# Performance work log

Hardware: AMD Instinct MI355X
Metric: run time of the kernel (lower is better)

The kernel has to match this reference:

```python
import jax, jax.numpy as jnp
import numpy as np

N = 50000
E = 1600000
NUM_GRAPHS = 64
NEG_SLOPE = 0.2


def _glorot(key, shape):
    fan_in, fan_out = shape[0], shape[-1]
    lim = jnp.sqrt(6.0 / (fan_in + fan_out))
    return jax.random.uniform(key, shape, jnp.float32, -lim, lim)


def setup_inputs() -> dict:
    key = jax.random.key(0)
    ks = jax.random.split(key, 16)
    x = jax.random.normal(ks[0], (N, 128), jnp.float32)
    edge_index = jax.random.randint(ks[1], (2, E), 0, N, jnp.int64)
    batch = jnp.sort(jax.random.randint(ks[2], (N,), 0, NUM_GRAPHS, jnp.int64))
    dims = [(128, 32), (32, 64), (64, 128)]
    params = {}
    for i, (fi, fo) in enumerate(dims, start=1):
        params[f'W{i}'] = _glorot(ks[3 * i], (fi, fo))
        params[f'a_src{i}'] = _glorot(ks[3 * i + 1], (1, fo))[0]
        params[f'a_dst{i}'] = _glorot(ks[3 * i + 2], (1, fo))[0]
        params[f'b{i}'] = jnp.zeros((fo,), jnp.float32)
    params['lin1_W'] = _glorot(ks[12], (128, 32))
    params['lin1_b'] = jnp.zeros((32,), jnp.float32)
    params['lin2_W'] = _glorot(ks[13], (32, 10))
    params['lin2_b'] = jnp.zeros((10,), jnp.float32)
    return dict(x=x, edge_index=edge_index, batch=batch, **params)


def gat_conv(x, src, dst, W, a_src, a_dst, b):
    # h: [N, F_out]
    h = x @ W
    # per-node attention logits, gathered per edge
    as_n = h @ a_src  # [N]
    ad_n = h @ a_dst  # [N]
    e = jax.nn.leaky_relu(as_n[src] + ad_n[dst], NEG_SLOPE)  # [E']
    # segment softmax over incoming edges of each destination node
    m = jax.ops.segment_max(e, dst, num_segments=N)
    ee = jnp.exp(e - m[dst])
    s = jax.ops.segment_sum(ee, dst, num_segments=N)
    alpha = ee / (s[dst] + 1e-16)
    # weighted scatter-add of source messages
    out = jax.ops.segment_sum(h[src] * alpha[:, None], dst, num_segments=N)
    return out + b


def reference(x, edge_index, batch, W1, a_src1, a_dst1, b1, W2, a_src2, a_dst2, b2,
              W3, a_src3, a_dst3, b3, lin1_W, lin1_b, lin2_W, lin2_b):
    # add self loops (PyG GATConv default)
    loops = jnp.arange(N, dtype=edge_index.dtype)
    src = jnp.concatenate([edge_index[0], loops])
    dst = jnp.concatenate([edge_index[1], loops])
    h = jax.nn.relu(gat_conv(x, src, dst, W1, a_src1, a_dst1, b1))
    h = jax.nn.relu(gat_conv(h, src, dst, W2, a_src2, a_dst2, b2))
    h = gat_conv(h, src, dst, W3, a_src3, a_dst3, b3)
    # global_add_pool over graphs
    g = jax.ops.segment_sum(h, batch, num_segments=NUM_GRAPHS)  # [G, 128]
    g = jax.nn.relu(g @ lin1_W + lin1_b)
    g = g @ lin2_W + lin2_b
    # faithful to original: log_softmax over dim=0 (batch axis)
    return jax.nn.log_softmax(g, axis=0)
```

## Files before the change

### kernel.cpp

```cpp
#include <hip/hip_runtime.h>
#include <cstdint>
#include <cstddef>

#define NN 50000
#define NE 1600000
#define NG 64
#define NCB 391
#define HB 98
#define EPB_A 8192
#define CAP_B 8192

__device__ __forceinline__ float bflo(unsigned u) { return __uint_as_float(u << 16); }
__device__ __forceinline__ float bfhi(unsigned u) { return __uint_as_float(u & 0xffff0000u); }
__device__ __forceinline__ unsigned f2bf(float f) {
    unsigned u = __float_as_uint(f);
    return (u + 0x7fffu + ((u >> 16) & 1u)) >> 16;
}
__device__ __forceinline__ float rdlane_f(float v, int l) {
    return __uint_as_float((unsigned)__builtin_amdgcn_readlane((int)__float_as_uint(v), l));
}

template <int FIN, int FOUT, bool HIST, bool ABF16>
__global__ void gemm_att_k(const void* __restrict__ Ain, const float* __restrict__ W,
                           const float* __restrict__ a_src, const float* __restrict__ a_dst,
                           unsigned* __restrict__ Hb, float* __restrict__ as_,
                           float* __restrict__ ad_, int gemmBlocks,
                           const int* __restrict__ edst, int* __restrict__ gcount) {
    __shared__ float Wl[FIN * FOUT];
    __shared__ float Al[32 * FIN];
    __shared__ int hh[NCB];
    int tid = threadIdx.x;
    if (HIST && blockIdx.x >= gemmBlocks) {
        int bid = blockIdx.x - gemmBlocks;
        for (int i = tid; i < NCB; i += 256) hh[i] = 0;
        __syncthreads();
        const int total4 = NE / 4;
        for (int i = bid * 256 + tid; i < total4; i += HB * 256) {
            int4 d = ((const int4*)edst)[i];
            atomicAdd(&hh[d.x >> 7], 1);
            atomicAdd(&hh[d.y >> 7], 1);
            atomicAdd(&hh[d.z >> 7], 1);
            atomicAdd(&hh[d.w >> 7], 1);
        }
        __syncthreads();
        for (int i = tid; i < NCB; i += 256)
            if (hh[i]) atomicAdd(&gcount[i], hh[i]);
        return;
    }
    const int RPB = 32;
    const int CP = FOUT / 2;
    const int CLANES = 256 / CP;
    const int RL = RPB / CLANES;
    for (int i = tid; i < (FIN * FOUT) / 4; i += 256)
        ((float4*)Wl)[i] = ((const float4*)W)[i];
    int rowbase = blockIdx.x * RPB;
    int nrows = min(RPB, NN - rowbase);
    int nel4 = (nrows * FIN) / 4;
    if (ABF16) {
        const ushort4* As = (const ushort4*)Ain + (size_t)rowbase * (FIN / 4);
        for (int i = tid; i < nel4; i += 256) {
            ushort4 u = As[i];
            ((float4*)Al)[i] = make_float4(bflo((unsigned)u.x), bflo((unsigned)u.y),
                                           bflo((unsigned)u.z), bflo((unsigned)u.w));
        }
    } else {
        const float4* As = (const float4*)Ain + (size_t)rowbase * (FIN / 4);
        for (int i = tid; i < nel4; i += 256) ((float4*)Al)[i] = As[i];
    }
    __syncthreads();
    int c2 = tid % CP;
    int rb = tid / CP;
    float acc0[RL], acc1[RL];
#pragma unroll
    for (int r = 0; r < RL; ++r) { acc0[r] = 0.f; acc1[r] = 0.f; }
#pragma unroll 4
    for (int k = 0; k < FIN; ++k) {
        float w0 = Wl[k * FOUT + 2 * c2];
        float w1 = Wl[k * FOUT + 2 * c2 + 1];
#pragma unroll
        for (int r = 0; r < RL; ++r) {
            float a = Al[(rb + r * CLANES) * FIN + k];
            acc0[r] += a * w0;
            acc1[r] += a * w1;
        }
    }
    float2 asrc2 = ((const float2*)a_src)[c2];
    float2 adst2 = ((const float2*)a_dst)[c2];
#pragma unroll
    for (int r = 0; r < RL; ++r) {
        int row = rowbase + rb + r * CLANES;
        float p1 = acc0[r] * asrc2.x + acc1[r] * asrc2.y;
        float p2 = acc0[r] * adst2.x + acc1[r] * adst2.y;
#pragma unroll
        for (int o = CP >> 1; o; o >>= 1) {
            p1 += __shfl_xor(p1, o, CP);
            p2 += __shfl_xor(p2, o, CP);
        }
        if (row < NN) {
            Hb[(size_t)row * CP + c2] = f2bf(acc0[r]) | (f2bf(acc1[r]) << 16);
            if (c2 == 0) { as_[row] = p1; ad_[row] = p2; }
        }
    }
}

__global__ void cscan_k(const int* __restrict__ gcount, int* __restrict__ cbase,
                        int* __restrict__ gcur) {
    __shared__ int part[256];
    int tid = threadIdx.x;
    int i0 = 2 * tid, i1 = 2 * tid + 1;
    int v0 = (i0 < NCB) ? gcount[i0] : 0;
    int v1 = (i1 < NCB) ? gcount[i1] : 0;
    part[tid] = v0 + v1;
    __syncthreads();
    for (int off = 1; off < 256; off <<= 1) {
        int v = (tid >= off) ? part[tid - off] : 0;
        __syncthreads();
        part[tid] += v;
        __syncthreads();
    }
    int run = tid ? part[tid - 1] : 0;
    if (i0 < NCB) { cbase[i0] = run; gcur[i0] = run; run += v0; }
    if (i1 < NCB) { cbase[i1] = run; gcur[i1] = run; run += v1; }
    if (tid == 255) cbase[NCB] = part[255];
}

__global__ void parta_k(const int* __restrict__ esrc, const int* __restrict__ edst,
                        int* __restrict__ gcur, int* __restrict__ pk_g) {
    __shared__ int cnt[NCB];
    __shared__ int base[NCB];
    __shared__ int cur[NCB];
    __shared__ int gposs[NCB];
    __shared__ int sc[256];
    __shared__ int lpk[EPB_A];
    int tid = threadIdx.x;
    int e0 = blockIdx.x * EPB_A;
    int e1 = min(e0 + EPB_A, NE);
    for (int i = tid; i < NCB; i += 256) cnt[i] = 0;
    __syncthreads();
    for (int i = e0 / 4 + tid; i < e1 / 4; i += 256) {
        int4 d = ((const int4*)edst)[i];
        atomicAdd(&cnt[d.x >> 7], 1);
        atomicAdd(&cnt[d.y >> 7], 1);
        atomicAdd(&cnt[d.z >> 7], 1);
        atomicAdd(&cnt[d.w >> 7], 1);
    }
    __syncthreads();
    int i0 = 2 * tid, i1 = 2 * tid + 1;
    int c0 = (i0 < NCB) ? cnt[i0] : 0;
    int c1 = (i1 < NCB) ? cnt[i1] : 0;
    sc[tid] = c0 + c1;
    __syncthreads();
    for (int off = 1; off < 256; off <<= 1) {
        int v = (tid >= off) ? sc[tid - off] : 0;
        __syncthreads();
        sc[tid] += v;
        __syncthreads();
    }
    int run = tid ? sc[tid - 1] : 0;
    if (i0 < NCB) {
        base[i0] = run; cur[i0] = run;
        gposs[i0] = atomicAdd(&gcur[i0], c0);
        run += c0;
    }
    if (i1 < NCB) {
        base[i1] = run; cur[i1] = run;
        gposs[i1] = atomicAdd(&gcur[i1], c1);
        run += c1;
    }
    __syncthreads();
    for (int i = e0 / 4 + tid; i < e1 / 4; i += 256) {
        int4 d = ((const int4*)edst)[i];
        int4 s = ((const int4*)esrc)[i];
        lpk[atomicAdd(&cur[d.x >> 7], 1)] = s.x | ((d.x & 127) << 17);
        lpk[atomicAdd(&cur[d.y >> 7], 1)] = s.y | ((d.y & 127) << 17);
        lpk[atomicAdd(&cur[d.z >> 7], 1)] = s.z | ((d.z & 127) << 17);
        lpk[atomicAdd(&cur[d.w >> 7], 1)] = s.w | ((d.w & 127) << 17);
    }
    __syncthreads();
    int wid = tid >> 6, lane = tid & 63;
    for (int c = wid; c < NCB; c += 4) {
        int n = cnt[c], gb = gposs[c], lb = base[c];
        for (int i = lane; i < n; i += 64) pk_g[gb + i] = lpk[lb + i];
    }
}

__global__ void partb_k(const int* __restrict__ pk_g, const int* __restrict__ cbase,
                        int* __restrict__ offsets, int* __restrict__ csr) {
    __shared__ int cnt[128];
    __shared__ int sc[256];
    __shared__ int lpk[CAP_B];
    int b = blockIdx.x, tid = threadIdx.x;
    int ebeg = cbase[b], eend = cbase[b + 1], n = eend - ebeg;
    int nbeg = b * 128;
    int ncnt = min(128, NN - nbeg);
    if (tid < 128) cnt[tid] = 0;
    __syncthreads();
    bool fits = (n <= CAP_B);
    if (fits) {
        for (int i = tid; i < n; i += 256) {
            int p = pk_g[ebeg + i];
            lpk[i] = p;
            atomicAdd(&cnt[p >> 17], 1);
        }
    } else {
        for (int i = tid; i < n; i += 256) atomicAdd(&cnt[pk_g[ebeg + i] >> 17], 1);
    }
    __syncthreads();
    int c0 = (tid < 128) ? cnt[tid] : 0;
    sc[tid] = c0;
    __syncthreads();
    for (int off = 1; off < 128; off <<= 1) {
        int v = (tid >= off && tid < 128) ? sc[tid - off] : 0;
        __syncthreads();
        if (tid < 128) sc[tid] += v;
        __syncthreads();
    }
    int excl = (tid < 128) ? sc[tid] - c0 : 0;
    if (tid < ncnt) offsets[nbeg + tid] = ebeg + excl;
    if (b == NCB - 1 && tid == 0) offsets[NN] = eend;
    __syncthreads();
    if (tid < 128) cnt[tid] = ebeg + excl;
    __syncthreads();
    if (fits) {
        for (int i = tid; i < n; i += 256) {
            int p = lpk[i];
            csr[atomicAdd(&cnt[p >> 17], 1)] = p & 0x1FFFF;
        }
    } else {
        for (int i = tid; i < n; i += 256) {
            int p = pk_g[ebeg + i];
            csr[atomicAdd(&cnt[p >> 17], 1)] = p & 0x1FFFF;
        }
    }
}

template <int F, bool RELU>
__global__ void node_agg_k(const int* __restrict__ off, const int* __restrict__ csr,
                           const float* __restrict__ as_, const float* __restrict__ ad_,
                           const unsigned* __restrict__ Hb2,
                           const float* __restrict__ b, unsigned* __restrict__ Ob) {
    int lane = threadIdx.x;
    int node = blockIdx.x;
    int beg = off[node], end = off[node + 1];
    float adn = ad_[node];
    float vself = as_[node] + adn;
    vself = vself > 0.f ? vself : 0.2f * vself;
    float eself = __expf(vself);
    float lsum = 0.f;

    if constexpr (F == 128) {
        unsigned hbs = Hb2[(size_t)node * 64 + lane];
        float accx = eself * bflo(hbs);
        float accy = eself * bfhi(hbs);
        for (int i0 = beg; i0 < end; i0 += 64) {
            int idx = i0 + lane;
            bool ok = idx < end;
            int s = ok ? csr[idx] : 0;
            float v = as_[s] + adn;
            v = v > 0.f ? v : 0.2f * v;
            float ee = ok ? __expf(v) : 0.f;
            lsum += ee;
            int rem = min(end - i0, 64);
            int j = 0;
            for (; j + 16 <= rem; j += 16) {
#pragma unroll
                for (int k = 0; k < 16; ++k) {
                    int s2 = __builtin_amdgcn_readlane(s, j + k);
                    float ee2 = rdlane_f(ee, j + k);
                    unsigned hb = (Hb2 + (size_t)s2 * 64)[lane];
                    accx += ee2 * bflo(hb);
                    accy += ee2 * bfhi(hb);
                }
            }
            for (; j + 4 <= rem; j += 4) {
#pragma unroll
                for (int k = 0; k < 4; ++k) {
                    int s2 = __builtin_amdgcn_readlane(s, j + k);
                    float ee2 = rdlane_f(ee, j + k);
                    unsigned hb = (Hb2 + (size_t)s2 * 64)[lane];
                    accx += ee2 * bflo(hb);
                    accy += ee2 * bfhi(hb);
                }
            }
            for (; j < rem; ++j) {
                int s2 = __builtin_amdgcn_readlane(s, j);
                float ee2 = rdlane_f(ee, j);
                unsigned hb = (Hb2 + (size_t)s2 * 64)[lane];
                accx += ee2 * bflo(hb);
                accy += ee2 * bfhi(hb);
            }
        }
#pragma unroll
        for (int o = 32; o; o >>= 1) lsum += __shfl_xor(lsum, o);
        float inv = 1.f / (lsum + eself + 1e-16f);
        float2 bb = ((const float2*)b)[lane];
        float ox = accx * inv + bb.x;
        float oy = accy * inv + bb.y;
        if (RELU) { ox = fmaxf(ox, 0.f); oy = fmaxf(oy, 0.f); }
        Ob[(size_t)node * 64 + lane] = f2bf(ox) | (f2bf(oy) << 16);
    } else if constexpr (F == 64) {
        int sg = lane >> 5;
        int cl = lane & 31;
        unsigned hbs = Hb2[(size_t)node * 32 + cl];
        float accx = (sg == 0) ? eself * bflo(hbs) : 0.f;
        float accy = (sg == 0) ? eself * bfhi(hbs) : 0.f;
        for (int i0 = beg; i0 < end; i0 += 64) {
            int idx = i0 + lane;
            bool ok = idx < end;
            int s = ok ? csr[idx] : 0;
            float v = as_[s] + adn;
            v = v > 0.f ? v : 0.2f * v;
            float ee = ok ? __expf(v) : 0.f;
            lsum += ee;
            int rem = min(end - i0, 64);
            int nj = (rem + 1) >> 1;
            nj = (nj + 3) & ~3;
            for (int j = 0; j < nj; j += 4) {
#pragma unroll
                for (int k = 0; k < 4; ++k) {
                    int pos = (j + k) * 2 + sg;
                    int s2 = __shfl(s, pos);
                    float ee2 = __shfl(ee, pos);
                    unsigned hb = Hb2[(size_t)s2 * 32 + cl];
                    accx += ee2 * bflo(hb);
                    accy += ee2 * bfhi(hb);
                }
            }
        }
#pragma unroll
        for (int o = 32; o; o >>= 1) lsum += __shfl_xor(lsum, o);
        float sum = lsum + eself;
        accx += __shfl_xor(accx, 32);
        accy += __shfl_xor(accy, 32);
        if (sg == 0) {
            float inv = 1.f / (sum + 1e-16f);
            float2 bb = ((const float2*)b)[cl];
            float ox = accx * inv + bb.x;
            float oy = accy * inv + bb.y;
            if (RELU) { ox = fmaxf(ox, 0.f); oy = fmaxf(oy, 0.f); }
            Ob[(size_t)node * 32 + cl] = f2bf(ox) | (f2bf(oy) << 16);
        }
    } else {
        const int GRP = 16, EPG = 4, U = 4;
        int sg = lane / GRP;
        int cl = lane % GRP;
        unsigned hbs = Hb2[(size_t)node * GRP + cl];
        float accx = (sg == 0) ? eself * bflo(hbs) : 0.f;
        float accy = (sg == 0) ? eself * bfhi(hbs) : 0.f;
        for (int i0 = beg; i0 < end; i0 += 64) {
            int idx = i0 + lane;
            bool ok = idx < end;
            int s = ok ? csr[idx] : 0;
            float v = as_[s] + adn;
            v = v > 0.f ? v : 0.2f * v;
            float ee = ok ? __expf(v) : 0.f;
            lsum += ee;
            int rem = min(end - i0, 64);
            int nj = (rem + EPG - 1) / EPG;
            nj = (nj + U - 1) & ~(U - 1);
            for (int j = 0; j < nj; j += U) {
#pragma unroll
                for (int k = 0; k < U; ++k) {
                    int pos = (j + k) * EPG + sg;
                    int s2 = __shfl(s, pos);
                    float ee2 = __shfl(ee, pos);
                    unsigned hb = Hb2[(size_t)s2 * GRP + cl];
                    accx += ee2 * bflo(hb);
                    accy += ee2 * bfhi(hb);
                }
            }
        }
#pragma unroll
        for (int o = 32; o; o >>= 1) lsum += __shfl_xor(lsum, o);
        float sum = lsum + eself;
#pragma unroll
        for (int o = 32; o >= GRP; o >>= 1) {
            accx += __shfl_xor(accx, o);
            accy += __shfl_xor(accy, o);
        }
        if (sg == 0) {
            float inv = 1.f / (sum + 1e-16f);
            float2 bb = ((const float2*)b)[cl];
            float ox = accx * inv + bb.x;
            float oy = accy * inv + bb.y;
            if (RELU) { ox = fmaxf(ox, 0.f); oy = fmaxf(oy, 0.f); }
            Ob[(size_t)node * GRP + cl] = f2bf(ox) | (f2bf(oy) << 16);
        }
    }
}

__global__ void pool_k(const unsigned* __restrict__ Ob, const int* __restrict__ batch,
                       float* __restrict__ g, int nodes_per_block) {
    __shared__ float acc[NG * 128];
    int c2 = threadIdx.x;
    for (int i = 0; i < NG; ++i) {
        acc[i * 128 + 2 * c2] = 0.f;
        acc[i * 128 + 2 * c2 + 1] = 0.f;
    }
    int start = blockIdx.x * nodes_per_block;
    int end = min(start + nodes_per_block, NN);
    int gmin = NG - 1, gmax = 0;
    for (int nd = start; nd < end; ++nd) {
        int gg = batch[nd];
        gmin = min(gmin, gg);
        gmax = max(gmax, gg);
        unsigned hb = Ob[(size_t)nd * 64 + c2];
        acc[gg * 128 + 2 * c2] += bflo(hb);
        acc[gg * 128 + 2 * c2 + 1] += bfhi(hb);
    }
    for (int i = gmin; i <= gmax; ++i) {
        atomicAdd(g + i * 128 + 2 * c2, acc[i * 128 + 2 * c2]);
        atomicAdd(g + i * 128 + 2 * c2 + 1, acc[i * 128 + 2 * c2 + 1]);
    }
}

__global__ void head_k(const float* __restrict__ g, const float* __restrict__ l1W,
                       const float* __restrict__ l1b, const float* __restrict__ l2W,
                       const float* __restrict__ l2b, float* __restrict__ out) {
    __shared__ float h1[NG * 32];
    __shared__ float o[NG * 10];
    int tid = threadIdx.x;
    for (int idx = tid; idx < NG * 32; idx += 256) {
        int r = idx / 32, c = idx % 32;
        float acc = l1b[c];
        for (int k = 0; k < 128; ++k) acc += g[r * 128 + k] * l1W[k * 32 + c];
        h1[idx] = fmaxf(acc, 0.f);
    }
    __syncthreads();
    for (int idx = tid; idx < NG * 10; idx += 256) {
        int r = idx / 10, c = idx % 10;
        float acc = l2b[c];
        for (int k = 0; k < 32; ++k) acc += h1[r * 32 + k] * l2W[k * 10 + c];
        o[idx] = acc;
    }
    __syncthreads();
    if (tid < 10) {
        float mx = -1e30f;
        for (int r = 0; r < NG; ++r) mx = fmaxf(mx, o[r * 10 + tid]);
        float sum = 0.f;
        for (int r = 0; r < NG; ++r) sum += __expf(o[r * 10 + tid] - mx);
        float lse = mx + logf(sum);
        for (int r = 0; r < NG; ++r) out[r * 10 + tid] = o[r * 10 + tid] - lse;
    }
}

extern "C" void kernel_launch(void* const* d_in, const int* in_sizes, int n_in,
                              void* d_out, int out_size, void* d_ws, size_t ws_size,
                              hipStream_t stream) {
    const float* x   = (const float*)d_in[0];
    const int* ei    = (const int*)d_in[1];
    const int* batch = (const int*)d_in[2];
    const float* W1 = (const float*)d_in[3];
    const float* as1 = (const float*)d_in[4];
    const float* ad1 = (const float*)d_in[5];
    const float* b1 = (const float*)d_in[6];
    const float* W2 = (const float*)d_in[7];
    const float* as2 = (const float*)d_in[8];
    const float* ad2 = (const float*)d_in[9];
    const float* b2 = (const float*)d_in[10];
    const float* W3 = (const float*)d_in[11];
    const float* as3 = (const float*)d_in[12];
    const float* ad3 = (const float*)d_in[13];
    const float* b3 = (const float*)d_in[14];
    const float* l1W = (const float*)d_in[15];
    const float* l1b = (const float*)d_in[16];
    const float* l2W = (const float*)d_in[17];
    const float* l2b = (const float*)d_in[18];
    float* out = (float*)d_out;

    const int* esrc = ei;
    const int* edst = ei + NE;

    char* ws = (char*)d_ws;
    unsigned* Hb  = (unsigned*)ws;
    unsigned* B0b = Hb + (size_t)NN * 64;
    unsigned* B1b = B0b + (size_t)NN * 16;
    unsigned* B2b = B1b + (size_t)NN * 32;
    float* as_ = (float*)(B2b + (size_t)NN * 64);
    float* ad_ = as_ + NN;
    int* gcount = (int*)(ad_ + NN);
    float* g    = (float*)(gcount + NCB);
    int* cbase  = (int*)(g + NG * 128);
    int* gcur   = cbase + NCB + 1;
    int* offsets = gcur + NCB + 2;
    int* csr    = offsets + NN + 1;
    int* pk     = csr + NE;
    const int GEMM_BLOCKS = (NN + 31) / 32;

    hipMemsetAsync(gcount, 0, (NCB + NG * 128) * 4, stream);

    gemm_att_k<128, 32, true, false><<<GEMM_BLOCKS + HB, 256, 0, stream>>>(
        x, W1, as1, ad1, Hb, as_, ad_, GEMM_BLOCKS, edst, gcount);
    cscan_k<<<1, 256, 0, stream>>>(gcount, cbase, gcur);
    parta_k<<<(NE + EPB_A - 1) / EPB_A, 256, 0, stream>>>(esrc, edst, gcur, pk);
    partb_k<<<NCB, 256, 0, stream>>>(pk, cbase, offsets, csr);
    node_agg_k<32, true><<<NN, 64, 0, stream>>>(offsets, csr, as_, ad_, Hb, b1, B0b);

    gemm_att_k<32, 64, false, true><<<GEMM_BLOCKS, 256, 0, stream>>>(
        B0b, W2, as2, ad2, Hb, as_, ad_, GEMM_BLOCKS, nullptr, nullptr);
    node_agg_k<64, true><<<NN, 64, 0, stream>>>(offsets, csr, as_, ad_, Hb, b2, B1b);

    gemm_att_k<64, 128, false, true><<<GEMM_BLOCKS, 256, 0, stream>>>(
        B1b, W3, as3, ad3, Hb, as_, ad_, GEMM_BLOCKS, nullptr, nullptr);
    node_agg_k<128, false><<<NN, 64, 0, stream>>>(offsets, csr, as_, ad_, Hb, b3, B2b);

    pool_k<<<(NN + 127) / 128, 64, 0, stream>>>(B2b, batch, g, 128);
    head_k<<<1, 256, 0, stream>>>(g, l1W, l1b, l2W, l2b, out);
}
```

Before: 291.3 us.

## Fuse next-layer GEMM and attention projections into node aggregation epilogue

The layer-2 and layer-3 dense transforms and their attention logits are now computed in the epilogue of the previous layer's per-node aggregation kernel. Each wavefront multiplies its aggregated row by the next weight matrix and writes the bf16 features plus the src/dst logits directly. This drops two GEMM launches and the round trip of the intermediate activations through global memory. In exchange, every node block reads the full weight matrix from global or cache instead of shared memory, and the per-node epilogue becomes heavier, with double-buffered logit arrays to avoid read/write hazards.

```diff
diff --git a/kernel.cpp b/kernel.cpp
--- a/kernel.cpp
+++ b/kernel.cpp
@@ -20,8 +20,8 @@
     return __uint_as_float((unsigned)__builtin_amdgcn_readlane((int)__float_as_uint(v), l));
 }
 
-template <int FIN, int FOUT, bool HIST, bool ABF16>
-__global__ void gemm_att_k(const void* __restrict__ Ain, const float* __restrict__ W,
+template <int FIN, int FOUT, bool HIST>
+__global__ void gemm_att_k(const float* __restrict__ Ain, const float* __restrict__ W,
                            const float* __restrict__ a_src, const float* __restrict__ a_dst,
                            unsigned* __restrict__ Hb, float* __restrict__ as_,
                            float* __restrict__ ad_, int gemmBlocks,
@@ -56,17 +56,8 @@
     int rowbase = blockIdx.x * RPB;
     int nrows = min(RPB, NN - rowbase);
     int nel4 = (nrows * FIN) / 4;
-    if (ABF16) {
-        const ushort4* As = (const ushort4*)Ain + (size_t)rowbase * (FIN / 4);
-        for (int i = tid; i < nel4; i += 256) {
-            ushort4 u = As[i];
-            ((float4*)Al)[i] = make_float4(bflo((unsigned)u.x), bflo((unsigned)u.y),
-                                           bflo((unsigned)u.z), bflo((unsigned)u.w));
-        }
-    } else {
-        const float4* As = (const float4*)Ain + (size_t)rowbase * (FIN / 4);
-        for (int i = tid; i < nel4; i += 256) ((float4*)Al)[i] = As[i];
-    }
+    const float4* As = (const float4*)Ain + (size_t)rowbase * (FIN / 4);
+    for (int i = tid; i < nel4; i += 256) ((float4*)Al)[i] = As[i];
     __syncthreads();
     int c2 = tid % CP;
     int rb = tid / CP;
@@ -234,29 +225,32 @@
     }
 }
 
-template <int F, bool RELU>
+template <int F, bool FUSE>
 __global__ void node_agg_k(const int* __restrict__ off, const int* __restrict__ csr,
-                           const float* __restrict__ as_, const float* __restrict__ ad_,
-                           const unsigned* __restrict__ Hb2,
-                           const float* __restrict__ b, unsigned* __restrict__ Ob) {
+                           const float* __restrict__ as_in, const float* __restrict__ ad_in,
+                           const unsigned* __restrict__ Hb_in, const float* __restrict__ b,
+                           unsigned* __restrict__ Ob,
+                           const float* __restrict__ Wn, const float* __restrict__ an_src,
+                           const float* __restrict__ an_dst, unsigned* __restrict__ Hb_out,
+                           float* __restrict__ as_out, float* __restrict__ ad_out) {
     int lane = threadIdx.x;
     int node = blockIdx.x;
     int beg = off[node], end = off[node + 1];
-    float adn = ad_[node];
-    float vself = as_[node] + adn;
+    float adn = ad_in[node];
+    float vself = as_in[node] + adn;
     vself = vself > 0.f ? vself : 0.2f * vself;
     float eself = __expf(vself);
     float lsum = 0.f;
 
     if constexpr (F == 128) {
-        unsigned hbs = Hb2[(size_t)node * 64 + lane];
+        unsigned hbs = Hb_in[(size_t)node * 64 + lane];
         float accx = eself * bflo(hbs);
         float accy = eself * bfhi(hbs);
         for (int i0 = beg; i0 < end; i0 += 64) {
             int idx = i0 + lane;
             bool ok = idx < end;
             int s = ok ? csr[idx] : 0;
-            float v = as_[s] + adn;
+            float v = as_in[s] + adn;
             v = v > 0.f ? v : 0.2f * v;
             float ee = ok ? __expf(v) : 0.f;
             lsum += ee;
@@ -267,7 +261,7 @@
                 for (int k = 0; k < 16; ++k) {
                     int s2 = __builtin_amdgcn_readlane(s, j + k);
                     float ee2 = rdlane_f(ee, j + k);
-                    unsigned hb = (Hb2 + (size_t)s2 * 64)[lane];
+                    unsigned hb = (Hb_in + (size_t)s2 * 64)[lane];
                     accx += ee2 * bflo(hb);
                     accy += ee2 * bfhi(hb);
                 }
@@ -277,7 +271,7 @@
                 for (int k = 0; k < 4; ++k) {
                     int s2 = __builtin_amdgcn_readlane(s, j + k);
                     float ee2 = rdlane_f(ee, j + k);
-                    unsigned hb = (Hb2 + (size_t)s2 * 64)[lane];
+                    unsigned hb = (Hb_in + (size_t)s2 * 64)[lane];
                     accx += ee2 * bflo(hb);
                     accy += ee2 * bfhi(hb);
                 }
@@ -285,7 +279,7 @@
             for (; j < rem; ++j) {
                 int s2 = __builtin_amdgcn_readlane(s, j);
                 float ee2 = rdlane_f(ee, j);
-                unsigned hb = (Hb2 + (size_t)s2 * 64)[lane];
+                unsigned hb = (Hb_in + (size_t)s2 * 64)[lane];
                 accx += ee2 * bflo(hb);
                 accy += ee2 * bfhi(hb);
             }
@@ -296,19 +290,18 @@
         float2 bb = ((const float2*)b)[lane];
         float ox = accx * inv + bb.x;
         float oy = accy * inv + bb.y;
-        if (RELU) { ox = fmaxf(ox, 0.f); oy = fmaxf(oy, 0.f); }
         Ob[(size_t)node * 64 + lane] = f2bf(ox) | (f2bf(oy) << 16);
     } else if constexpr (F == 64) {
         int sg = lane >> 5;
         int cl = lane & 31;
-        unsigned hbs = Hb2[(size_t)node * 32 + cl];
+        unsigned hbs = Hb_in[(size_t)node * 32 + cl];
         float accx = (sg == 0) ? eself * bflo(hbs) : 0.f;
         float accy = (sg == 0) ? eself * bfhi(hbs) : 0.f;
         for (int i0 = beg; i0 < end; i0 += 64) {
             int idx = i0 + lane;
             bool ok = idx < end;
             int s = ok ? csr[idx] : 0;
-            float v = as_[s] + adn;
+            float v = as_in[s] + adn;
             v = v > 0.f ? v : 0.2f * v;
             float ee = ok ? __expf(v) : 0.f;
             lsum += ee;
@@ -321,7 +314,7 @@
                     int pos = (j + k) * 2 + sg;
                     int s2 = __shfl(s, pos);
                     float ee2 = __shfl(ee, pos);
-                    unsigned hb = Hb2[(size_t)s2 * 32 + cl];
+                    unsigned hb = Hb_in[(size_t)s2 * 32 + cl];
                     accx += ee2 * bflo(hb);
                     accy += ee2 * bfhi(hb);
                 }
@@ -332,26 +325,43 @@
         float sum = lsum + eself;
         accx += __shfl_xor(accx, 32);
         accy += __shfl_xor(accy, 32);
-        if (sg == 0) {
-            float inv = 1.f / (sum + 1e-16f);
-            float2 bb = ((const float2*)b)[cl];
-            float ox = accx * inv + bb.x;
-            float oy = accy * inv + bb.y;
-            if (RELU) { ox = fmaxf(ox, 0.f); oy = fmaxf(oy, 0.f); }
-            Ob[(size_t)node * 32 + cl] = f2bf(ox) | (f2bf(oy) << 16);
-        }
+        float inv = 1.f / (sum + 1e-16f);
+        float2 bb = ((const float2*)b)[cl];
+        float ox = fmaxf(accx * inv + bb.x, 0.f);
+        float oy = fmaxf(accy * inv + bb.y, 0.f);
+        float hx = 0.f, hy = 0.f;
+#pragma unroll 8
+        for (int k = 0; k < 32; ++k) {
+            float bx = __shfl(ox, k);
+            float by = __shfl(oy, k);
+            float2 w0 = ((const float2*)(Wn + (size_t)(2 * k) * 128))[lane];
+            float2 w1 = ((const float2*)(Wn + (size_t)(2 * k + 1) * 128))[lane];
+            hx += bx * w0.x + by * w1.x;
+            hy += bx * w0.y + by * w1.y;
+        }
+        float2 s2v = ((const float2*)an_src)[lane];
+        float2 d2v = ((const float2*)an_dst)[lane];
+        float p1 = hx * s2v.x + hy * s2v.y;
+        float p2 = hx * d2v.x + hy * d2v.y;
+#pragma unroll
+        for (int o = 32; o; o >>= 1) {
+            p1 += __shfl_xor(p1, o);
+            p2 += __shfl_xor(p2, o);
+        }
+        if (lane == 0) { as_out[node] = p1; ad_out[node] = p2; }
+        Hb_out[(size_t)node * 64 + lane] = f2bf(hx) | (f2bf(hy) << 16);
     } else {
         const int GRP = 16, EPG = 4, U = 4;
         int sg = lane / GRP;
         int cl = lane % GRP;
-        unsigned hbs = Hb2[(size_t)node * GRP + cl];
+        unsigned hbs = Hb_in[(size_t)node * GRP + cl];
         float accx = (sg == 0) ? eself * bflo(hbs) : 0.f;
         float accy = (sg == 0) ? eself * bfhi(hbs) : 0.f;
         for (int i0 = beg; i0 < end; i0 += 64) {
             int idx = i0 + lane;
             bool ok = idx < end;
             int s = ok ? csr[idx] : 0;
-            float v = as_[s] + adn;
+            float v = as_in[s] + adn;
             v = v > 0.f ? v : 0.2f * v;
             float ee = ok ? __expf(v) : 0.f;
             lsum += ee;
@@ -364,7 +374,7 @@
                     int pos = (j + k) * EPG + sg;
                     int s2 = __shfl(s, pos);
                     float ee2 = __shfl(ee, pos);
-                    unsigned hb = Hb2[(size_t)s2 * GRP + cl];
+                    unsigned hb = Hb_in[(size_t)s2 * GRP + cl];
                     accx += ee2 * bflo(hb);
                     accy += ee2 * bfhi(hb);
                 }
@@ -378,14 +388,29 @@
             accx += __shfl_xor(accx, o);
             accy += __shfl_xor(accy, o);
         }
-        if (sg == 0) {
-            float inv = 1.f / (sum + 1e-16f);
-            float2 bb = ((const float2*)b)[cl];
-            float ox = accx * inv + bb.x;
-            float oy = accy * inv + bb.y;
-            if (RELU) { ox = fmaxf(ox, 0.f); oy = fmaxf(oy, 0.f); }
-            Ob[(size_t)node * GRP + cl] = f2bf(ox) | (f2bf(oy) << 16);
-        }
+        float inv = 1.f / (sum + 1e-16f);
+        float2 bb = ((const float2*)b)[cl];
+        float ox = fmaxf(accx * inv + bb.x, 0.f);
+        float oy = fmaxf(accy * inv + bb.y, 0.f);
+        float hn = 0.f;
+#pragma unroll 8
+        for (int k = 0; k < 16; ++k) {
+            float bx = __shfl(ox, k);
+            float by = __shfl(oy, k);
+            hn += bx * Wn[(size_t)(2 * k) * 64 + lane];
+            hn += by * Wn[(size_t)(2 * k + 1) * 64 + lane];
+        }
+        float p1 = hn * an_src[lane];
+        float p2 = hn * an_dst[lane];
+#pragma unroll
+        for (int o = 32; o; o >>= 1) {
+            p1 += __shfl_xor(p1, o);
+            p2 += __shfl_xor(p2, o);
+        }
+        if (lane == 0) { as_out[node] = p1; ad_out[node] = p2; }
+        unsigned hb16 = f2bf(hn);
+        unsigned other = __shfl(hb16, lane | 1);
+        if (!(lane & 1)) Hb_out[(size_t)node * 32 + (lane >> 1)] = hb16 | (other << 16);
     }
 }
 
@@ -472,13 +497,15 @@
     const int* edst = ei + NE;
 
     char* ws = (char*)d_ws;
-    unsigned* Hb  = (unsigned*)ws;
-    unsigned* B0b = Hb + (size_t)NN * 64;
-    unsigned* B1b = B0b + (size_t)NN * 16;
-    unsigned* B2b = B1b + (size_t)NN * 32;
-    float* as_ = (float*)(B2b + (size_t)NN * 64);
-    float* ad_ = as_ + NN;
-    int* gcount = (int*)(ad_ + NN);
+    unsigned* Hb1 = (unsigned*)ws;
+    unsigned* Hb2 = Hb1 + (size_t)NN * 16;
+    unsigned* Hb3 = Hb2 + (size_t)NN * 32;
+    unsigned* B2b = Hb3 + (size_t)NN * 64;
+    float* asA = (float*)(B2b + (size_t)NN * 64);
+    float* adA = asA + NN;
+    float* asB = adA + NN;
+    float* adB = asB + NN;
+    int* gcount = (int*)(adB + NN);
     float* g    = (float*)(gcount + NCB);
     int* cbase  = (int*)(g + NG * 128);
     int* gcur   = cbase + NCB + 1;
@@ -489,20 +516,19 @@
 
     hipMemsetAsync(gcount, 0, (NCB + NG * 128) * 4, stream);
 
-    gemm_att_k<128, 32, true, false><<<GEMM_BLOCKS + HB, 256, 0, stream>>>(
-        x, W1, as1, ad1, Hb, as_, ad_, GEMM_BLOCKS, edst, gcount);
+    gemm_att_k<128, 32, true><<<GEMM_BLOCKS + HB, 256, 0, stream>>>(
+        x, W1, as1, ad1, Hb1, asA, adA, GEMM_BLOCKS, edst, gcount);
     cscan_k<<<1, 256, 0, stream>>>(gcount, cbase, gcur);
     parta_k<<<(NE + EPB_A - 1) / EPB_A, 256, 0, stream>>>(esrc, edst, gcur, pk);
     partb_k<<<NCB, 256, 0, stream>>>(pk, cbase, offsets, csr);
-    node_agg_k<32, true><<<NN, 64, 0, stream>>>(offsets, csr, as_, ad_, Hb, b1, B0b);
-
-    gemm_att_k<32, 64, false, true><<<GEMM_BLOCKS, 256, 0, stream>>>(
-        B0b, W2, as2, ad2, Hb, as_, ad_, GEMM_BLOCKS, nullptr, nullptr);
-    node_agg_k<64, true><<<NN, 64, 0, stream>>>(offsets, csr, as_, ad_, Hb, b2, B1b);
-
-    gemm_att_k<64, 128, false, true><<<GEMM_BLOCKS, 256, 0, stream>>>(
-        B1b, W3, as3, ad3, Hb, as_, ad_, GEMM_BLOCKS, nullptr, nullptr);
-    node_agg_k<128, false><<<NN, 64, 0, stream>>>(offsets, csr, as_, ad_, Hb, b3, B2b);
+
+    node_agg_k<32, true><<<NN, 64, 0, stream>>>(offsets, csr, asA, adA, Hb1, b1,
+                                                nullptr, W2, as2, ad2, Hb2, asB, adB);
+    node_agg_k<64, true><<<NN, 64, 0, stream>>>(offsets, csr, asB, adB, Hb2, b2,
+                                                nullptr, W3, as3, ad3, Hb3, asA, adA);
+    node_agg_k<128, false><<<NN, 64, 0, stream>>>(offsets, csr, asA, adA, Hb3, b3,
+                                                  B2b, nullptr, nullptr, nullptr,
+                                                  nullptr, nullptr, nullptr);
 
     pool_k<<<(NN + 127) / 128, 64, 0, stream>>>(B2b, batch, g, 128);
     head_k<<<1, 256, 0, stream>>>(g, l1W, l1b, l2W, l2b, out);
```

Result: slower. 349.3 us (median of 2 runs) (+19.9%).
